# Kernel optimization log

Hardware: AMD Instinct MI355X
Metric: run time of the kernel (lower is better)

## Reference

```python
import jax, jax.numpy as jnp
import numpy as np

N, D = 4096, 1024

def setup_inputs() -> dict:
    key = jax.random.key(0)
    ks = jax.random.split(key, 7)
    s = 1.0 / np.sqrt(D)
    return {
        "x": jax.random.normal(ks[0], (N, D), dtype=jnp.float32),
        "Wq": jax.random.uniform(ks[1], (D, D), jnp.float32, -s, s),
        "bq": jax.random.uniform(ks[2], (D,), jnp.float32, -s, s),
        "Wk": jax.random.uniform(ks[3], (D, D), jnp.float32, -s, s),
        "bk": jax.random.uniform(ks[4], (D,), jnp.float32, -s, s),
        "Wv": jax.random.uniform(ks[5], (D, D), jnp.float32, -s, s),
        "bv": jax.random.uniform(ks[6], (D,), jnp.float32, -s, s),
    }

def reference(x, Wq, bq, Wk, bk, Wv, bv):
    # Linear layers: y = x @ W^T + b (torch convention, W is [out, in]; here square)
    Q = x @ Wq.T + bq  # [N, D]
    K = x @ Wk.T + bk  # [N, D]
    V = x @ Wv.T + bv  # [N, D]
    scores = (Q @ K.T) / jnp.sqrt(jnp.asarray(x.shape[-1], x.dtype))  # [N, N]
    attn = jax.nn.softmax(scores, axis=-1)
    return attn @ V  # [N, D]
```

## Files before the change

kernel.cpp:

```cpp
#include <hip/hip_runtime.h>


#define N_TOK 4096
#define DDIM  1024

typedef short s16x4 __attribute__((ext_vector_type(4)));
typedef short s16x8 __attribute__((ext_vector_type(8)));
typedef float f32x4 __attribute__((ext_vector_type(4)));

#define VMCNT0() asm volatile("s_waitcnt vmcnt(0)" ::: "memory")
#define VMCNT8() asm volatile("s_waitcnt vmcnt(8)" ::: "memory")
#define LGKMCNT0() asm volatile("s_waitcnt lgkmcnt(0)" ::: "memory")
#define BARRIER() do { asm volatile("" ::: "memory"); \
                       __builtin_amdgcn_s_barrier();  \
                       asm volatile("" ::: "memory"); } while (0)

__device__ inline short f2b(float f) {
  unsigned int u = __float_as_uint(f);
  unsigned int r = (u + 0x7FFFu + ((u >> 16) & 1u)) >> 16;
  return (short)(unsigned short)r;
}

__device__ __forceinline__ void gld_lds16(const short* g, short* l) {
  __builtin_amdgcn_global_load_lds(
      (const __attribute__((address_space(1))) unsigned int*)g,
      (__attribute__((address_space(3))) unsigned int*)l, 16, 0, 0);
}

__device__ __forceinline__ void xcd_remap(int gx, int& bx, int& by) {
  const int L = by * gx + bx;
  const int g = L & 7, h = L >> 3;
  by = g * 4 + (h & 3);
  bx = h >> 2;
}
__device__ __forceinline__ void xcd_remap16(int gx, int& bx, int& by) {
  const int L = by * gx + bx;
  const int g = L & 7, h = L >> 3;
  by = g * 2 + (h & 1);
  bx = h >> 1;
}

template<int BM, int BN, int BK, int MODE>
constexpr int lds_shorts() {
  return (MODE == 3 && BN * 136 > BM * BK + BN * BK) ? BN * 136
                                                     : BM * BK + BN * BK;
}

template<int BM, int BN, int BK, int MODE>
__device__ __forceinline__ void gemm_core(
    const short* __restrict__ A, const short* __restrict__ B,
    void* __restrict__ C, float* __restrict__ aux, short* smem,
    int K, int ld, int ldc, float scale, int row0, int col0)
{
  constexpr int WM = BM / 2, WN = BN / 2, AI = WM / 16, AJ = WN / 16;
  constexpr int CPR = BK / 8;
  constexpr int MASK = CPR - 1;
  constexpr int CA = BM * CPR / 256;
  constexpr int CB = BN * CPR / 256;
  constexpr int NH = BK / 32;
  short* As = smem;
  short* Bs = smem + BM * BK;

  const int tid  = threadIdx.x;
  const int wave = tid >> 6, lane = tid & 63;
  const int wm = wave >> 1, wn = wave & 1;
  const int quad = lane >> 4, lr = lane & 15;

  f32x4 acc[AI][AJ];
  #pragma unroll
  for (int i = 0; i < AI; i++)
    #pragma unroll
    for (int j = 0; j < AJ; j++) acc[i][j] = {0.f, 0.f, 0.f, 0.f};

  for (int kk = 0; kk < K; kk += BK) {
    __syncthreads();
    #pragma unroll
    for (int c = 0; c < CA; c++) {
      const int id = c * 256 + wave * 64 + lane;
      const int r = id / CPR, slot = id & MASK;
      const int q = slot ^ (r & MASK);
      gld_lds16(A + (size_t)(row0 + r) * ld + kk + q * 8,
                &As[(c * 256 + wave * 64) * 8]);
    }
    #pragma unroll
    for (int c = 0; c < CB; c++) {
      const int id = c * 256 + wave * 64 + lane;
      const int r = id / CPR, slot = id & MASK;
      const int q = slot ^ (r & MASK);
      gld_lds16(B + (size_t)(col0 + r) * ld + kk + q * 8,
                &Bs[(c * 256 + wave * 64) * 8]);
    }
    __syncthreads();

    #pragma unroll
    for (int h = 0; h < NH; h++) {
      s16x8 af[AI], bf[AJ];
      #pragma unroll
      for (int i = 0; i < AI; i++) {
        const int row = wm * WM + i * 16 + lr;
        const int ch = (h * 4 + quad) ^ (row & MASK);
        af[i] = *reinterpret_cast<const s16x8*>(&As[(row * CPR + ch) * 8]);
      }
      #pragma unroll
      for (int j = 0; j < AJ; j++) {
        const int row = wn * WN + j * 16 + lr;
        const int ch = (h * 4 + quad) ^ (row & MASK);
        bf[j] = *reinterpret_cast<const s16x8*>(&Bs[(row * CPR + ch) * 8]);
      }
      #pragma unroll
      for (int i = 0; i < AI; i++)
        #pragma unroll
        for (int j = 0; j < AJ; j++)
          acc[i][j] = __builtin_amdgcn_mfma_f32_16x16x32_bf16(af[i], bf[j], acc[i][j], 0, 0, 0);
    }
  }

  if constexpr (MODE == 0) {
    float bb[AJ];
    #pragma unroll
    for (int j = 0; j < AJ; j++) bb[j] = aux[col0 + wn * WN + j * 16 + lr];
    #pragma unroll
    for (int i = 0; i < AI; i++) {
      const int r0 = row0 + wm * WM + i * 16 + quad * 4;
      #pragma unroll
      for (int j = 0; j < AJ; j++) {
        const int c = col0 + wn * WN + j * 16 + lr;
        #pragma unroll
        for (int r = 0; r < 4; r++)
          ((short*)C)[(size_t)(r0 + r) * ldc + c] = f2b(acc[i][j][r] * scale + bb[j]);
      }
    }
  } else if constexpr (MODE == 2) {
    #pragma unroll
    for (int i = 0; i < AI; i++) {
      const int r0 = row0 + wm * WM + i * 16 + quad * 4;
      float linv[4];
      #pragma unroll
      for (int r = 0; r < 4; r++) linv[r] = 1.0f / aux[r0 + r];
      #pragma unroll
      for (int j = 0; j < AJ; j++) {
        const int c = col0 + wn * WN + j * 16 + lr;
        #pragma unroll
        for (int r = 0; r < 4; r++)
          ((float*)C)[(size_t)(r0 + r) * ldc + c] = acc[i][j][r] * linv[r];
      }
    }
  } else {
    float bb[AJ];
    #pragma unroll
    for (int j = 0; j < AJ; j++) bb[j] = aux[col0 + wn * WN + j * 16 + lr];
    __syncthreads();
    short* trans = smem;
    #pragma unroll
    for (int i = 0; i < AI; i++) {
      const int rl = wm * WM + i * 16 + quad * 4;
      #pragma unroll
      for (int j = 0; j < AJ; j++) {
        const int cl = wn * WN + j * 16 + lr;
        s16x4 v;
        #pragma unroll
        for (int r = 0; r < 4; r++) v[r] = f2b(acc[i][j][r] * scale + bb[j]);
        *reinterpret_cast<s16x4*>(&trans[cl * 136 + rl]) = v;
      }
    }
    __syncthreads();
    #pragma unroll
    for (int s = 0; s < BM * BN / 8 / 256; s++) {
      const int u = s * 256 + tid;
      const int cc = u >> (31 - __builtin_clz(BM / 8));
      const int seg = u & (BM / 8 - 1);
      s16x8 v = *reinterpret_cast<const s16x8*>(&trans[cc * 136 + seg * 8]);
      *reinterpret_cast<s16x8*>(
          &((short*)C)[(size_t)(cc + col0) * ldc + row0 + seg * 8]) = v;
    }
  }
}

#define XU  (N_TOK * DDIM / 8)
#define WU  (DDIM * DDIM / 8)
#define NCVT ((XU + 3 * WU) / 256)
__global__ __launch_bounds__(256)
void cvt_all(const float* __restrict__ x,  const float* __restrict__ wq,
             const float* __restrict__ wk, const float* __restrict__ wv,
             short* __restrict__ xb, short* __restrict__ wqb,
             short* __restrict__ wkb, short* __restrict__ wvb,
             float* __restrict__ rowsum)
{
  if (blockIdx.x >= NCVT) {
    float4 z = {0.f, 0.f, 0.f, 0.f};
    float4* p = reinterpret_cast<float4*>(rowsum) + threadIdx.x * 4;
    p[0] = z; p[1] = z; p[2] = z; p[3] = z;
    return;
  }
  int gid = blockIdx.x * 256 + threadIdx.x;
  const float* src; short* dst; int off;
  if (gid < XU)               { src = x;  dst = xb;  off = gid; }
  else if (gid < XU + WU)     { src = wq; dst = wqb; off = gid - XU; }
  else if (gid < XU + 2 * WU) { src = wk; dst = wkb; off = gid - XU - WU; }
  else                        { src = wv; dst = wvb; off = gid - XU - 2 * WU; }
  const float4* g = reinterpret_cast<const float4*>(src) + (size_t)off * 2;
  float4 a = g[0], b = g[1];
  s16x8 o;
  o[0] = f2b(a.x); o[1] = f2b(a.y); o[2] = f2b(a.z); o[3] = f2b(a.w);
  o[4] = f2b(b.x); o[5] = f2b(b.y); o[6] = f2b(b.z); o[7] = f2b(b.w);
  reinterpret_cast<s16x8*>(dst)[off] = o;
}

__global__ __launch_bounds__(256)
void k_qkv(const short* __restrict__ xb,
           const short* __restrict__ Wqb, const short* __restrict__ Wkb,
           const short* __restrict__ Wvb,
           const float* __restrict__ bq, const float* __restrict__ bk,
           const float* __restrict__ bv,
           short* __restrict__ Qb, short* __restrict__ Kb, short* __restrict__ Vt)
{
  __shared__ short smem[lds_shorts<128, 128, 64, 3>()];
  int bx = blockIdx.x, by = blockIdx.y;
  xcd_remap(DDIM / 128, bx, by);
  if (blockIdx.z == 0) {
    gemm_core<128, 128, 64, 0>(xb, Wqb, Qb, (float*)bq, smem, DDIM, DDIM, DDIM,
                               1.0f, by * 128, bx * 128);
  } else if (blockIdx.z == 1) {
    gemm_core<128, 128, 64, 0>(xb, Wkb, Kb, (float*)bk, smem, DDIM, DDIM, DDIM,
                               1.0f, by * 128, bx * 128);
  } else {
    gemm_core<128, 128, 64, 3>(xb, Wvb, Vt, (float*)bv, smem, DDIM, DDIM, N_TOK,
                               1.0f, by * 128, bx * 128);
  }
}

__global__ __launch_bounds__(256, 2)
void k_score(const short* __restrict__ Qb, const short* __restrict__ Kb,
             short* __restrict__ SP, float* __restrict__ rowsum)
{
  constexpr int BM = 128, BN = 128, BK = 64;
  constexpr int NT = DDIM / BK;
  __shared__ short smem[2][(BM + BN) * BK];

  int bx = blockIdx.x, by = blockIdx.y;
  xcd_remap(32, bx, by);
  const int row0 = by * BM, col0 = bx * BN;

  const int tid  = threadIdx.x;
  const int wave = tid >> 6, lane = tid & 63;
  const int wm = wave >> 1, wn = wave & 1;
  const int quad = lane >> 4, lr = lane & 15;

  auto stage = [&](int t, int sl) {
    #pragma unroll
    for (int c = 0; c < 8; c++) {
      const int id = c * 256 + tid;
      const int r  = id >> 3;
      const int q  = (id & 7) ^ (r & 7);
      const short* src = (r < BM)
          ? Qb + (size_t)(row0 + r) * DDIM + t * BK + q * 8
          : Kb + (size_t)(col0 + r - BM) * DDIM + t * BK + q * 8;
      gld_lds16(src, &smem[sl][(c * 256 + wave * 64) * 8]);
    }
  };

  f32x4 acc[4][4];
  #pragma unroll
  for (int i = 0; i < 4; i++)
    #pragma unroll
    for (int j = 0; j < 4; j++) acc[i][j] = {0.f, 0.f, 0.f, 0.f};

  stage(0, 0);
  stage(1, 1);
  VMCNT8();
  BARRIER();

  for (int t = 0; t < NT; t++) {
    const int sl = t & 1;
    const short* As = smem[sl];
    const short* Bs = smem[sl] + BM * BK;

    s16x8 af[2][4], bf[2][4];
    #pragma unroll
    for (int h = 0; h < 2; h++) {
      #pragma unroll
      for (int i = 0; i < 4; i++) {
        const int row = wm * 64 + i * 16 + lr;
        const int ch = (h * 4 + quad) ^ (row & 7);
        af[h][i] = *reinterpret_cast<const s16x8*>(&As[(row * 8 + ch) * 8]);
      }
      #pragma unroll
      for (int j = 0; j < 4; j++) {
        const int row = wn * 64 + j * 16 + lr;
        const int ch = (h * 4 + quad) ^ (row & 7);
        bf[h][j] = *reinterpret_cast<const s16x8*>(&Bs[(row * 8 + ch) * 8]);
      }
    }
    LGKMCNT0();
    __builtin_amdgcn_sched_barrier(0);
    BARRIER();

    const bool pf = (t + 2) < NT;
    if (pf) stage(t + 2, sl);

    __builtin_amdgcn_s_setprio(1);
    #pragma unroll
    for (int h = 0; h < 2; h++)
      #pragma unroll
      for (int i = 0; i < 4; i++)
        #pragma unroll
        for (int j = 0; j < 4; j++)
          acc[i][j] = __builtin_amdgcn_mfma_f32_16x16x32_bf16(
              af[h][i], bf[h][j], acc[i][j], 0, 0, 0);
    __builtin_amdgcn_s_setprio(0);

    if (pf) { VMCNT8(); } else { VMCNT0(); }
    BARRIER();
  }

  constexpr float scale = 0.03125f;
  #pragma unroll
  for (int i = 0; i < 4; i++) {
    const int r0 = row0 + wm * 64 + i * 16 + quad * 4;
    float ex[4][4];
    #pragma unroll
    for (int j = 0; j < 4; j++) {
      const int c = col0 + wn * 64 + j * 16 + lr;
      #pragma unroll
      for (int r = 0; r < 4; r++) {
        ex[j][r] = __expf(acc[i][j][r] * scale);
        SP[(size_t)(r0 + r) * N_TOK + c] = f2b(ex[j][r]);
      }
    }
    #pragma unroll
    for (int r = 0; r < 4; r++) {
      float s = 0.f;
      #pragma unroll
      for (int j = 0; j < 4; j++) s += ex[j][r];
      s += __shfl_xor(s, 1, 64);
      s += __shfl_xor(s, 2, 64);
      s += __shfl_xor(s, 4, 64);
      s += __shfl_xor(s, 8, 64);
      if (lr == 0) atomicAdd(&rowsum[r0 + r], s);
    }
  }
}

__global__ __launch_bounds__(256)
void k_pv(const short* __restrict__ SP, const short* __restrict__ Vt,
          float* __restrict__ out, const float* __restrict__ rowsum)
{
  __shared__ short smem[lds_shorts<128, 64, 128, 2>()];
  int bx = blockIdx.x, by = blockIdx.y;
  xcd_remap(DDIM / 64, bx, by);
  gemm_core<128, 64, 128, 2>(SP, Vt, out, (float*)rowsum, smem, N_TOK, N_TOK,
                             DDIM, 1.0f, by * 128, bx * 64);
}

extern "C" void kernel_launch(void* const* d_in, const int* in_sizes, int n_in,
                              void* d_out, int out_size, void* d_ws, size_t ws_size,
                              hipStream_t stream)
{
  const float* x  = (const float*)d_in[0];
  const float* Wq = (const float*)d_in[1];
  const float* bq = (const float*)d_in[2];
  const float* Wk = (const float*)d_in[3];
  const float* bk = (const float*)d_in[4];
  const float* Wv = (const float*)d_in[5];
  const float* bv = (const float*)d_in[6];
  float* out = (float*)d_out;

  char* ws = (char*)d_ws;
  const size_t MB = 1024 * 1024;
  short* Qb  = (short*)(ws + 0 * MB);
  short* Kb  = (short*)(ws + 8 * MB);
  short* Vt  = (short*)(ws + 24 * MB);
  short* SP  = (short*)(ws + 32 * MB);
  short* xb  = (short*)(ws + 32 * MB);
  short* Wqb = (short*)(ws + 40 * MB);
  short* Wkb = (short*)(ws + 42 * MB);
  short* Wvb = (short*)(ws + 44 * MB);
  float* rowsum = (float*)(ws + 64 * MB);

  dim3 b256(256);

  cvt_all<<<dim3(NCVT + 1), b256, 0, stream>>>(
      x, Wq, Wk, Wv, xb, Wqb, Wkb, Wvb, rowsum);

  k_qkv<<<dim3(DDIM / 128, N_TOK / 128, 3), b256, 0, stream>>>(
      xb, Wqb, Wkb, Wvb, bq, bk, bv, Qb, Kb, Vt);

  k_score<<<dim3(32, 32), b256, 0, stream>>>(Qb, Kb, SP, rowsum);

  k_pv<<<dim3(DDIM / 64, N_TOK / 128), b256, 0, stream>>>(
      SP, Vt, out, rowsum);
}
```

Before: 207.1 us.

## Replace PV GEMM with dedicated double-buffered BK=64 swizzled kernel

The attention-times-V kernel stops using the generic gemm_core and gets its own loop. It uses a 64-wide K tile with two LDS stages loaded asynchronously through global_load_lds, an XOR swizzle to avoid bank conflicts, and prefetch issued right after the fragment reads so loads overlap the MFMAs. It also asks for two blocks per CU through launch_bounds, raises wave priority around the MFMA block, and folds the row-sum normalization into its epilogue. The smaller LDS footprint is meant to improve occupancy and latency hiding, at the cost of more barriers per K step.

```diff
diff --git a/kernel.cpp b/kernel.cpp
--- a/kernel.cpp
+++ b/kernel.cpp
@@ -9,6 +9,7 @@
 typedef float f32x4 __attribute__((ext_vector_type(4)));
 
 #define VMCNT0() asm volatile("s_waitcnt vmcnt(0)" ::: "memory")
+#define VMCNT6() asm volatile("s_waitcnt vmcnt(6)" ::: "memory")
 #define VMCNT8() asm volatile("s_waitcnt vmcnt(8)" ::: "memory")
 #define LGKMCNT0() asm volatile("s_waitcnt lgkmcnt(0)" ::: "memory")
 #define BARRIER() do { asm volatile("" ::: "memory"); \
@@ -128,21 +129,6 @@
         #pragma unroll
         for (int r = 0; r < 4; r++)
           ((short*)C)[(size_t)(r0 + r) * ldc + c] = f2b(acc[i][j][r] * scale + bb[j]);
-      }
-    }
-  } else if constexpr (MODE == 2) {
-    #pragma unroll
-    for (int i = 0; i < AI; i++) {
-      const int r0 = row0 + wm * WM + i * 16 + quad * 4;
-      float linv[4];
-      #pragma unroll
-      for (int r = 0; r < 4; r++) linv[r] = 1.0f / aux[r0 + r];
-      #pragma unroll
-      for (int j = 0; j < AJ; j++) {
-        const int c = col0 + wn * WN + j * 16 + lr;
-        #pragma unroll
-        for (int r = 0; r < 4; r++)
-          ((float*)C)[(size_t)(r0 + r) * ldc + c] = acc[i][j][r] * linv[r];
       }
     }
   } else {
@@ -341,15 +327,104 @@
   }
 }
 
-__global__ __launch_bounds__(256)
+__global__ __launch_bounds__(256, 2)
 void k_pv(const short* __restrict__ SP, const short* __restrict__ Vt,
           float* __restrict__ out, const float* __restrict__ rowsum)
 {
-  __shared__ short smem[lds_shorts<128, 64, 128, 2>()];
+  constexpr int BM = 128, BN = 64, BK = 64;
+  constexpr int NT = N_TOK / BK;
+  __shared__ short smem[2][(BM + BN) * BK];
+
   int bx = blockIdx.x, by = blockIdx.y;
   xcd_remap(DDIM / 64, bx, by);
-  gemm_core<128, 64, 128, 2>(SP, Vt, out, (float*)rowsum, smem, N_TOK, N_TOK,
-                             DDIM, 1.0f, by * 128, bx * 64);
+  const int row0 = by * BM, col0 = bx * BN;
+
+  const int tid  = threadIdx.x;
+  const int wave = tid >> 6, lane = tid & 63;
+  const int wm = wave >> 1, wn = wave & 1;
+  const int quad = lane >> 4, lr = lane & 15;
+
+  auto stage = [&](int t, int sl) {
+    #pragma unroll
+    for (int c = 0; c < 6; c++) {
+      const int id = c * 256 + tid;
+      const int r  = id >> 3;
+      const int q  = (id & 7) ^ (r & 7);
+      const short* src = (r < BM)
+          ? SP + (size_t)(row0 + r) * N_TOK + t * BK + q * 8
+          : Vt + (size_t)(col0 + r - BM) * N_TOK + t * BK + q * 8;
+      gld_lds16(src, &smem[sl][(c * 256 + wave * 64) * 8]);
+    }
+  };
+
+  f32x4 acc[4][2];
+  #pragma unroll
+  for (int i = 0; i < 4; i++)
+    #pragma unroll
+    for (int j = 0; j < 2; j++) acc[i][j] = {0.f, 0.f, 0.f, 0.f};
+
+  stage(0, 0);
+  stage(1, 1);
+  VMCNT6();
+  BARRIER();
+
+  for (int t = 0; t < NT; t++) {
+    const int sl = t & 1;
+    const short* As = smem[sl];
+    const short* Bs = smem[sl] + BM * BK;
+
+    s16x8 af[2][4], bf[2][2];
+    #pragma unroll
+    for (int h = 0; h < 2; h++) {
+      #pragma unroll
+      for (int i = 0; i < 4; i++) {
+        const int row = wm * 64 + i * 16 + lr;
+        const int ch = (h * 4 + quad) ^ (row & 7);
+        af[h][i] = *reinterpret_cast<const s16x8*>(&As[(row * 8 + ch) * 8]);
+      }
+      #pragma unroll
+      for (int j = 0; j < 2; j++) {
+        const int row = wn * 32 + j * 16 + lr;
+        const int ch = (h * 4 + quad) ^ (row & 7);
+        bf[h][j] = *reinterpret_cast<const s16x8*>(&Bs[(row * 8 + ch) * 8]);
+      }
+    }
+    LGKMCNT0();
+    __builtin_amdgcn_sched_barrier(0);
+    BARRIER();
+
+    const bool pf = (t + 2) < NT;
+    if (pf) stage(t + 2, sl);
+
+    __builtin_amdgcn_s_setprio(1);
+    #pragma unroll
+    for (int h = 0; h < 2; h++)
+      #pragma unroll
+      for (int i = 0; i < 4; i++)
+        #pragma unroll
+        for (int j = 0; j < 2; j++)
+          acc[i][j] = __builtin_amdgcn_mfma_f32_16x16x32_bf16(
+              af[h][i], bf[h][j], acc[i][j], 0, 0, 0);
+    __builtin_amdgcn_s_setprio(0);
+
+    if (pf) { VMCNT6(); } else { VMCNT0(); }
+    BARRIER();
+  }
+
+  #pragma unroll
+  for (int i = 0; i < 4; i++) {
+    const int r0 = row0 + wm * 64 + i * 16 + quad * 4;
+    float linv[4];
+    #pragma unroll
+    for (int r = 0; r < 4; r++) linv[r] = 1.0f / rowsum[r0 + r];
+    #pragma unroll
+    for (int j = 0; j < 2; j++) {
+      const int c = col0 + wn * 32 + j * 16 + lr;
+      #pragma unroll
+      for (int r = 0; r < 4; r++)
+        out[(size_t)(r0 + r) * DDIM + c] = acc[i][j][r] * linv[r];
+    }
+  }
 }
 
 extern "C" void kernel_launch(void* const* d_in, const int* in_sizes, int n_in,
```

New measurement: 200.0 us. 1.04x faster.
